# Optimization experiments

Hardware: AMD Instinct MI355X
Metric: run time of the kernel (lower is better)

The kernel has to match this reference:

```python
import jax, jax.numpy as jnp
import numpy as np

EPS = 1e-5  # torch BatchNorm1d default eps


def _bn(y2d, g, b):
    # BatchNorm1d in training mode: biased batch stats over axis 0
    m = y2d.mean(axis=0)
    v = y2d.var(axis=0)
    return (y2d - m) * jax.lax.rsqrt(v + EPS) * g + b


def setup_inputs() -> dict:
    key = jax.random.key(0)
    ks = jax.random.split(key, 18)
    S, B, D, H, O = 1000, 64, 440, 512, 1000
    u = lambda k, shape, n: jax.random.uniform(k, shape, jnp.float32, -1.0 / np.sqrt(n), 1.0 / np.sqrt(n))
    fin = np.sqrt(0.01 / (H + O))
    return {
        "x": jax.random.normal(ks[0], (S, B, D), jnp.float32),
        "Wh": u(ks[1], (H, D), D),
        "Wz": u(ks[2], (H, D), D),
        "Wr": u(ks[3], (H, D), D),
        "Uh": u(ks[4], (H, H), H),
        "Uz": u(ks[5], (H, H), H),
        "Ur": u(ks[6], (H, H), H),
        "gh": 1.0 + 0.1 * jax.random.normal(ks[7], (H,), jnp.float32),
        "bh": 0.1 * jax.random.normal(ks[8], (H,), jnp.float32),
        "gz": 1.0 + 0.1 * jax.random.normal(ks[9], (H,), jnp.float32),
        "bz": 0.1 * jax.random.normal(ks[10], (H,), jnp.float32),
        "gr": 1.0 + 0.1 * jax.random.normal(ks[11], (H,), jnp.float32),
        "br": 0.1 * jax.random.normal(ks[12], (H,), jnp.float32),
        "Wf": jax.random.uniform(ks[13], (O, H), jnp.float32, -fin, fin),
        "gf": 1.0 + 0.1 * jax.random.normal(ks[14], (O,), jnp.float32),
        "bf": 0.1 * jax.random.normal(ks[15], (O,), jnp.float32),
    }


def reference(x, Wh, Wz, Wr, Uh, Uz, Ur, gh, bh, gz, bz, gr, br, Wf, gf, bf):
    S, B, D = x.shape
    H = Wh.shape[0]
    xf = x.reshape(S * B, D)
    # gate input projections (no bias; BN in train mode over flattened (S*B, H))
    wh = _bn(xf @ Wh.T, gh, bh).reshape(S, B, H)
    wz = _bn(xf @ Wz.T, gz, bz).reshape(S, B, H)
    wr = _bn(xf @ Wr.T, gr, br).reshape(S, B, H)

    def step(ht, gates):
        whk, wzk, wrk = gates
        zt = jax.nn.sigmoid(wzk + ht @ Uz.T)
        rt = jax.nn.sigmoid(wrk + ht @ Ur.T)
        hcand = jnp.tanh(whk + (rt * ht) @ Uh.T)  # drop_mask==1 (gru_drop=0.0)
        ht = zt * ht + (1.0 - zt) * hcand
        return ht, ht

    h0 = jnp.zeros((B, H), x.dtype)
    _, h = jax.lax.scan(step, h0, (wh, wz, wr))  # h: (S, B, H)

    ws = _bn(h.reshape(S * B, H) @ Wf.T, gf, bf)
    return jax.nn.log_softmax(ws, axis=1)
```

## Files before the change

### kernel.cpp

```cpp
#include <hip/hip_runtime.h>
#include <cstdint>

typedef unsigned short u16;
typedef __attribute__((ext_vector_type(8))) short bf16x8;
typedef __attribute__((ext_vector_type(4))) float f32x4;

#define S_LEN 1000
#define NWG   32

#define OFF_HALL   0ull
#define SZ_HALL    (1001ull*64*512*2)
#define OFF_WCAT   (OFF_HALL + SZ_HALL)
#define SZ_WCAT    (1536ull*448*2)
#define OFF_WFB    (OFF_WCAT + SZ_WCAT)
#define SZ_WFB     (1024ull*512*2)
#define OFF_RH     (OFF_WFB + SZ_WFB)
#define SZ_RH      (64ull*512*2)
#define OFF_GSUM   (OFF_RH + SZ_RH)
#define OFF_GSQ    (OFF_GSUM + 1536*4)
#define OFF_AALL   (OFF_GSQ  + 1536*4)
#define OFF_CALL   (OFF_AALL + 1536*4)
#define OFF_SSUM   (OFF_CALL + 1536*4)
#define OFF_SSQ    (OFF_SSUM + 1024*4)
#define OFF_AF     (OFF_SSQ  + 1024*4)
#define OFF_CF     (OFF_AF   + 1024*4)
#define OFF_FLAGS  (OFF_CF   + 1024*4)
#define STATS_ZERO_BYTES (OFF_FLAGS + 256 - OFF_GSUM)

__device__ __forceinline__ float bf2f(u16 u) {
  union { unsigned u; float f; } v; v.u = ((unsigned)u) << 16; return v.f;
}
__device__ __forceinline__ u16 f2bf(float f) {
  union { float f; unsigned u; } v; v.f = f;
  unsigned r = (v.u + 0x7fffu + ((v.u >> 16) & 1u)) >> 16;
  return (u16)r;
}
__device__ __forceinline__ float sigm(float x) { return 1.f / (1.f + __expf(-x)); }
__device__ __forceinline__ float tanh_(float x) {
  float e = __expf(-2.f * fabsf(x));
  float r = (1.f - e) / (1.f + e);
  return x >= 0.f ? r : -r;
}

__device__ __forceinline__ void stage16(const u16* g, u16* l) {
#if defined(__has_builtin) && __has_builtin(__builtin_amdgcn_global_load_lds)
  __builtin_amdgcn_global_load_lds((const __attribute__((address_space(1))) unsigned int*)(g),
                                   (__attribute__((address_space(3))) unsigned int*)(l), 16, 0, 0);
#else
  int lane = threadIdx.x & 63;
  *(bf16x8*)(l + lane * 8) = *(const bf16x8*)(g + lane * 0);
#endif
}

__global__ void cvt_pad(const float* __restrict__ src, u16* __restrict__ dst, int incols, int outcols) {
  int r = blockIdx.x, ci = threadIdx.x;
  float v = (ci < incols) ? src[(size_t)r * incols + ci] : 0.f;
  dst[(size_t)r * outcols + ci] = f2bf(v);
}
__global__ void cvt_wf(const float* __restrict__ src, u16* __restrict__ dst) {
  int r = blockIdx.x, ci = threadIdx.x;
  float v = (r < 1000) ? src[(size_t)r * 512 + ci] : 0.f;
  dst[(size_t)r * 512 + ci] = f2bf(v);
}

template<bool F32OUT>
__global__ __launch_bounds__(256, 1) void gemm_bt(const u16* __restrict__ A, const u16* __restrict__ B,
                                                  void* __restrict__ Cout, int K, int ldc, int nlimit) {
  __shared__ __align__(16) u16 smem[16 * 512];
  const int bm = blockIdx.x * 128;
  const int bn = blockIdx.y * 128;
  const int tid = threadIdx.x;
  const int w = tid >> 6;
  const int lane = tid & 63;
  const int r = lane & 15;
  const int q = lane >> 4;
  const int wm = w & 1, wn = w >> 1;

  f32x4 acc[4][4];
#pragma unroll
  for (int i = 0; i < 4; ++i)
#pragma unroll
    for (int j = 0; j < 4; ++j) acc[i][j] = (f32x4){0.f, 0.f, 0.f, 0.f};

  const u16* gA0 = A + (size_t)(bm + w * 16 + r) * K + q * 8;
  const u16* gA1 = A + (size_t)(bm + (w + 4) * 16 + r) * K + q * 8;
  const u16* gB0 = B + (size_t)(bn + w * 16 + r) * K + q * 8;
  const u16* gB1 = B + (size_t)(bn + (w + 4) * 16 + r) * K + q * 8;
  u16* As = smem;
  u16* Bs = smem + 8 * 512;

  for (int k0 = 0; k0 < K; k0 += 32) {
    stage16(gA0 + k0, As + w * 512);
    stage16(gA1 + k0, As + (w + 4) * 512);
    stage16(gB0 + k0, Bs + w * 512);
    stage16(gB1 + k0, Bs + (w + 4) * 512);
    __syncthreads();
    bf16x8 af[4], bf_[4];
#pragma unroll
    for (int mi = 0; mi < 4; ++mi) af[mi] = *(const bf16x8*)(As + (wm * 4 + mi) * 512 + lane * 8);
#pragma unroll
    for (int ni = 0; ni < 4; ++ni) bf_[ni] = *(const bf16x8*)(Bs + (wn * 4 + ni) * 512 + lane * 8);
#pragma unroll
    for (int mi = 0; mi < 4; ++mi)
#pragma unroll
      for (int ni = 0; ni < 4; ++ni)
        acc[mi][ni] = __builtin_amdgcn_mfma_f32_16x16x32_bf16(af[mi], bf_[ni], acc[mi][ni], 0, 0, 0);
    __syncthreads();
  }
  const int row0 = bm + wm * 64;
  const int col0 = bn + wn * 64;
#pragma unroll
  for (int mi = 0; mi < 4; ++mi)
#pragma unroll
    for (int ni = 0; ni < 4; ++ni)
#pragma unroll
      for (int i = 0; i < 4; ++i) {
        int rr = row0 + mi * 16 + q * 4 + i;
        int cc = col0 + ni * 16 + r;
        if (F32OUT) {
          if (cc < nlimit) ((float*)Cout)[(size_t)rr * ldc + cc] = acc[mi][ni][i];
        } else {
          ((u16*)Cout)[(size_t)rr * ldc + cc] = f2bf(acc[mi][ni][i]);
        }
      }
}

template<int BF16IN>
__global__ __launch_bounds__(256, 1) void colstats(const void* __restrict__ Xv, int ld, int ncols,
                                                   float* __restrict__ sum, float* __restrict__ sumsq) {
  const int col = blockIdx.x * 128 + (threadIdx.x & 127);
  const int half = threadIdx.x >> 7;
  const int r0 = blockIdx.y * 2000;
  float s = 0.f, ss = 0.f;
  if (col < ncols) {
    if (BF16IN) {
      const u16* X = (const u16*)Xv;
      for (int rr = r0 + half; rr < r0 + 2000; rr += 2) {
        float v = bf2f(X[(size_t)rr * ld + col]); s += v; ss += v * v;
      }
    } else {
      const float* X = (const float*)Xv;
      for (int rr = r0 + half; rr < r0 + 2000; rr += 2) {
        float v = X[(size_t)rr * ld + col]; s += v; ss += v * v;
      }
    }
  }
  __shared__ float ls[128], lss[128];
  if (half) { ls[threadIdx.x & 127] = s; lss[threadIdx.x & 127] = ss; }
  __syncthreads();
  if (!half && col < ncols) {
    s += ls[threadIdx.x]; ss += lss[threadIdx.x];
    atomicAdd(&sum[col], s); atomicAdd(&sumsq[col], ss);
  }
}

__global__ void fin_gate(const float* __restrict__ sum, const float* __restrict__ sq,
                         const float* gh, const float* bh, const float* gz, const float* bz,
                         const float* gr, const float* br, float* __restrict__ a, float* __restrict__ c) {
  int j = blockIdx.x * 256 + threadIdx.x;
  if (j >= 1536) return;
  float m = sum[j] * (1.f / 64000.f);
  float v = sq[j] * (1.f / 64000.f) - m * m;
  int seg = j >> 9, jj = j & 511;
  float gg = seg == 0 ? gh[jj] : seg == 1 ? gz[jj] : gr[jj];
  float bb = seg == 0 ? bh[jj] : seg == 1 ? bz[jj] : br[jj];
  float aa = gg * rsqrtf(v + 1e-5f);
  a[j] = aa; c[j] = bb - m * aa;
}

__global__ void fin_score(const float* __restrict__ sum, const float* __restrict__ sq,
                          const float* __restrict__ gfp, const float* __restrict__ bfp,
                          float* __restrict__ a, float* __restrict__ c) {
  int j = blockIdx.x * 256 + threadIdx.x;
  if (j >= 1000) return;
  float m = sum[j] * (1.f / 64000.f);
  float v = sq[j] * (1.f / 64000.f) - m * m;
  float aa = gfp[j] * rsqrtf(v + 1e-5f);
  a[j] = aa; c[j] = bfp[j] - m * aa;
}

__device__ __forceinline__ void gbar(unsigned* cnt, unsigned* gen, unsigned n) {
  __syncthreads();
  if (threadIdx.x == 0) {
    __builtin_amdgcn_fence(__ATOMIC_RELEASE, "agent");
    unsigned prev = __hip_atomic_fetch_add(cnt, 1u, __ATOMIC_ACQ_REL, __HIP_MEMORY_SCOPE_AGENT);
    if (prev == n * NWG - 1u) {
      __hip_atomic_store(gen, n, __ATOMIC_RELEASE, __HIP_MEMORY_SCOPE_AGENT);
    } else {
      while (__hip_atomic_load(gen, __ATOMIC_ACQUIRE, __HIP_MEMORY_SCOPE_AGENT) < n)
        __builtin_amdgcn_s_sleep(1);
    }
    __builtin_amdgcn_fence(__ATOMIC_ACQUIRE, "agent");
  }
  __syncthreads();
}

__global__ __launch_bounds__(256, 1) void scan_kernel(
    const u16* __restrict__ gates,
    const float* __restrict__ Uz, const float* __restrict__ Ur, const float* __restrict__ Uh,
    const float* __restrict__ acoef, const float* __restrict__ ccoef,
    u16* __restrict__ hall,
    u16* __restrict__ rh,
    unsigned* __restrict__ bcnt, unsigned* __restrict__ bgen) {
  __shared__ __align__(16) u16 Us[3][16][520];
  __shared__ float co[6][16];
  const int g = blockIdx.x;
  const int j0 = g * 16;
  const int tid = threadIdx.x;
  const int w = tid >> 6;
  const int lane = tid & 63;
  const int r = lane & 15;
  const int q = lane >> 4;

  for (int idx = tid; idx < 3 * 16 * 512; idx += 256) {
    int u = idx >> 13;
    int rem = idx & 8191;
    int j = rem >> 9;
    int k = rem & 511;
    const float* U = (u == 0) ? Uz : (u == 1) ? Ur : Uh;
    Us[u][j][k] = f2bf(U[(size_t)(j0 + j) * 512 + k]);
  }
  if (tid < 16) {
    co[0][tid] = acoef[512 + j0 + tid];  co[1][tid] = ccoef[512 + j0 + tid];
    co[2][tid] = acoef[1024 + j0 + tid]; co[3][tid] = ccoef[1024 + j0 + tid];
    co[4][tid] = acoef[j0 + tid];        co[5][tid] = ccoef[j0 + tid];
  }
  __syncthreads();
  const float az = co[0][r], cz = co[1][r], ar = co[2][r], cr = co[3][r];
  const float ah = co[4][r], ch = co[5][r];

  unsigned bn_ = 0;
  for (int t = 1; t <= S_LEN; ++t) {
    const u16* hprev = hall + (size_t)(t - 1) * (64 * 512);
    f32x4 accz = {0.f, 0.f, 0.f, 0.f}, accr = {0.f, 0.f, 0.f, 0.f};
    const u16* arow = hprev + (size_t)(w * 16 + r) * 512 + q * 8;
#pragma unroll
    for (int ks = 0; ks < 16; ++ks) {
      bf16x8 a = *(const bf16x8*)(arow + ks * 32);
      bf16x8 bz = *(const bf16x8*)(&Us[0][r][ks * 32 + q * 8]);
      bf16x8 br2 = *(const bf16x8*)(&Us[1][r][ks * 32 + q * 8]);
      accz = __builtin_amdgcn_mfma_f32_16x16x32_bf16(a, bz, accz, 0, 0, 0);
      accr = __builtin_amdgcn_mfma_f32_16x16x32_bf16(a, br2, accr, 0, 0, 0);
    }
    const size_t grow = (size_t)(t - 1) * 64 + w * 16 + q * 4;
    float zv[4], rv[4], hp[4];
#pragma unroll
    for (int i = 0; i < 4; ++i) {
      float wz = bf2f(gates[(grow + i) * 1536 + 512 + j0 + r]);
      float wr = bf2f(gates[(grow + i) * 1536 + 1024 + j0 + r]);
      zv[i] = sigm(accz[i] + wz * az + cz);
      rv[i] = sigm(accr[i] + wr * ar + cr);
      hp[i] = bf2f(hprev[(size_t)(w * 16 + q * 4 + i) * 512 + j0 + r]);
      rh[(size_t)(w * 16 + q * 4 + i) * 512 + j0 + r] = f2bf(rv[i] * hp[i]);
    }
    gbar(bcnt, bgen, ++bn_);
    f32x4 acch = {0.f, 0.f, 0.f, 0.f};
    const u16* rrow = rh + (size_t)(w * 16 + r) * 512 + q * 8;
#pragma unroll
    for (int ks = 0; ks < 16; ++ks) {
      bf16x8 a = *(const bf16x8*)(rrow + ks * 32);
      bf16x8 bh = *(const bf16x8*)(&Us[2][r][ks * 32 + q * 8]);
      acch = __builtin_amdgcn_mfma_f32_16x16x32_bf16(a, bh, acch, 0, 0, 0);
    }
    u16* hnew = hall + (size_t)t * (64 * 512);
#pragma unroll
    for (int i = 0; i < 4; ++i) {
      float wh = bf2f(gates[(grow + i) * 1536 + j0 + r]);
      float hc = tanh_(acch[i] + wh * ah + ch);
      float hn = zv[i] * hp[i] + (1.f - zv[i]) * hc;
      hnew[(size_t)(w * 16 + q * 4 + i) * 512 + j0 + r] = f2bf(hn);
    }
    gbar(bcnt, bgen, ++bn_);
  }
}

__global__ __launch_bounds__(256, 1) void logsoftmax_k(float* __restrict__ S,
                                                       const float* __restrict__ a, const float* __restrict__ c) {
  __shared__ float as_[1000], cs_[1000];
  for (int i = threadIdx.x; i < 1000; i += 256) { as_[i] = a[i]; cs_[i] = c[i]; }
  __syncthreads();
  const int w = threadIdx.x >> 6, lane = threadIdx.x & 63;
  for (int it = 0; it < 4; ++it) {
    const int row = blockIdx.x * 16 + it * 4 + w;
    float* Srow = S + (size_t)row * 1000;
    float tv[16];
    float mx = -3.0e38f;
#pragma unroll
    for (int qq = 0; qq < 16; ++qq) {
      int j = lane + qq * 64;
      float v = -3.0e38f;
      if (j < 1000) v = as_[j] * Srow[j] + cs_[j];
      tv[qq] = v;
      mx = fmaxf(mx, v);
    }
#pragma unroll
    for (int o = 32; o > 0; o >>= 1) mx = fmaxf(mx, __shfl_xor(mx, o));
    float sm = 0.f;
#pragma unroll
    for (int qq = 0; qq < 16; ++qq) sm += __expf(tv[qq] - mx);
#pragma unroll
    for (int o = 32; o > 0; o >>= 1) sm += __shfl_xor(sm, o);
    float lse = mx + __logf(sm);
#pragma unroll
    for (int qq = 0; qq < 16; ++qq) {
      int j = lane + qq * 64;
      if (j < 1000) Srow[j] = tv[qq] - lse;
    }
  }
}

extern "C" void kernel_launch(void* const* d_in, const int* in_sizes, int n_in,
                              void* d_out, int out_size, void* d_ws, size_t ws_size,
                              hipStream_t stream) {
  const float* x  = (const float*)d_in[0];
  const float* Wh = (const float*)d_in[1];
  const float* Wz = (const float*)d_in[2];
  const float* Wr = (const float*)d_in[3];
  const float* Uh = (const float*)d_in[4];
  const float* Uz = (const float*)d_in[5];
  const float* Ur = (const float*)d_in[6];
  const float* gh = (const float*)d_in[7];
  const float* bh = (const float*)d_in[8];
  const float* gz = (const float*)d_in[9];
  const float* bz = (const float*)d_in[10];
  const float* gr = (const float*)d_in[11];
  const float* br = (const float*)d_in[12];
  const float* Wf = (const float*)d_in[13];
  const float* gf = (const float*)d_in[14];
  const float* bfp = (const float*)d_in[15];

  uint8_t* ws = (uint8_t*)d_ws;
  u16* hall = (u16*)(ws + OFF_HALL);
  u16* xb   = (u16*)(ws + OFF_HALL);
  u16* wcat = (u16*)(ws + OFF_WCAT);
  u16* wfb  = (u16*)(ws + OFF_WFB);
  u16* rh   = (u16*)(ws + OFF_RH);
  float* gsum = (float*)(ws + OFF_GSUM);
  float* gsq  = (float*)(ws + OFF_GSQ);
  float* aall = (float*)(ws + OFF_AALL);
  float* call = (float*)(ws + OFF_CALL);
  float* ssum = (float*)(ws + OFF_SSUM);
  float* ssq  = (float*)(ws + OFF_SSQ);
  float* af   = (float*)(ws + OFF_AF);
  float* cf   = (float*)(ws + OFF_CF);
  unsigned* flags = (unsigned*)(ws + OFF_FLAGS);

  u16* gates = (u16*)d_out;
  float* scores = (float*)d_out;

  hipMemsetAsync(ws + OFF_GSUM, 0, (size_t)STATS_ZERO_BYTES, stream);

  cvt_pad<<<dim3(64000), dim3(448), 0, stream>>>(x, xb, 440, 448);
  cvt_pad<<<dim3(512), dim3(448), 0, stream>>>(Wh, wcat, 440, 448);
  cvt_pad<<<dim3(512), dim3(448), 0, stream>>>(Wz, wcat + 512 * 448, 440, 448);
  cvt_pad<<<dim3(512), dim3(448), 0, stream>>>(Wr, wcat + 1024 * 448, 440, 448);
  cvt_wf<<<dim3(1024), dim3(512), 0, stream>>>(Wf, wfb);

  gemm_bt<false><<<dim3(500, 12), dim3(256), 0, stream>>>(xb, wcat, (void*)gates, 448, 1536, 1536);

  colstats<1><<<dim3(12, 32), dim3(256), 0, stream>>>((const void*)gates, 1536, 1536, gsum, gsq);
  fin_gate<<<dim3(6), dim3(256), 0, stream>>>(gsum, gsq, gh, bh, gz, bz, gr, br, aall, call);

  hipMemsetAsync(ws + OFF_HALL, 0, (size_t)(64 * 512 * 2), stream);

  scan_kernel<<<dim3(NWG), dim3(256), 0, stream>>>(gates, Uz, Ur, Uh, aall, call, hall, rh,
                                                   flags, flags + 32);

  gemm_bt<true><<<dim3(500, 8), dim3(256), 0, stream>>>(hall + 64 * 512, wfb, (void*)scores, 512, 1000, 1000);

  colstats<0><<<dim3(8, 32), dim3(256), 0, stream>>>((const void*)scores, 1000, 1000, ssum, ssq);
  fin_score<<<dim3(4), dim3(256), 0, stream>>>(ssum, ssq, gf, bfp, af, cf);

  logsoftmax_k<<<dim3(4000), dim3(256), 0, stream>>>(scores, af, cf);
}
```

Measured before the change: 13.64 ms.

## Replace scan grid barrier with per-block flags and transpose gate layout

Swaps the counter-based grid barrier in the recurrent scan for per-workgroup flag publishing: each block writes its own flag and one wavefront polls all 32 flags. h and r*h are now exchanged through relaxed agent-scope atomics, stores are packed in pairs, and the previous h is kept in registers instead of being reloaded. The gate GEMM now writes a transposed gates layout so each lane reads its four timestep gates with one 8-byte load. BN stats for the gates become a row reduction that needs no atomics. The risk is memory-ordering correctness, since relaxed atomics plus s_waitcnt replace explicit fences.

```diff
diff --git a/kernel.cpp b/kernel.cpp
--- a/kernel.cpp
+++ b/kernel.cpp
@@ -2,6 +2,7 @@
 #include <cstdint>
 
 typedef unsigned short u16;
+typedef unsigned long long u64;
 typedef __attribute__((ext_vector_type(8))) short bf16x8;
 typedef __attribute__((ext_vector_type(4))) float f32x4;
 
@@ -25,7 +26,7 @@
 #define OFF_AF     (OFF_SSQ  + 1024*4)
 #define OFF_CF     (OFF_AF   + 1024*4)
 #define OFF_FLAGS  (OFF_CF   + 1024*4)
-#define STATS_ZERO_BYTES (OFF_FLAGS + 256 - OFF_GSUM)
+#define STATS_ZERO_BYTES (OFF_FLAGS + 2048 - OFF_SSUM)
 
 __device__ __forceinline__ float bf2f(u16 u) {
   union { unsigned u; float f; } v; v.u = ((unsigned)u) << 16; return v.f;
@@ -42,14 +43,17 @@
   return x >= 0.f ? r : -r;
 }
 
+__device__ __forceinline__ u64 ld8(const u16* p) {
+  return __hip_atomic_load((const u64*)p, __ATOMIC_RELAXED, __HIP_MEMORY_SCOPE_AGENT);
+}
+__device__ __forceinline__ void st4(u16* p, unsigned v) {
+  __hip_atomic_store((unsigned*)p, v, __ATOMIC_RELAXED, __HIP_MEMORY_SCOPE_AGENT);
+}
+union Frag { u64 q[2]; bf16x8 v; };
+
 __device__ __forceinline__ void stage16(const u16* g, u16* l) {
-#if defined(__has_builtin) && __has_builtin(__builtin_amdgcn_global_load_lds)
   __builtin_amdgcn_global_load_lds((const __attribute__((address_space(1))) unsigned int*)(g),
                                    (__attribute__((address_space(3))) unsigned int*)(l), 16, 0, 0);
-#else
-  int lane = threadIdx.x & 63;
-  *(bf16x8*)(l + lane * 8) = *(const bf16x8*)(g + lane * 0);
-#endif
 }
 
 __global__ void cvt_pad(const float* __restrict__ src, u16* __restrict__ dst, int incols, int outcols) {
@@ -63,7 +67,7 @@
   dst[(size_t)r * 512 + ci] = f2bf(v);
 }
 
-template<bool F32OUT>
+template<int MODE>
 __global__ __launch_bounds__(256, 1) void gemm_bt(const u16* __restrict__ A, const u16* __restrict__ B,
                                                   void* __restrict__ Cout, int K, int ldc, int nlimit) {
   __shared__ __align__(16) u16 smem[16 * 512];
@@ -112,37 +116,52 @@
 #pragma unroll
   for (int mi = 0; mi < 4; ++mi)
 #pragma unroll
-    for (int ni = 0; ni < 4; ++ni)
-#pragma unroll
-      for (int i = 0; i < 4; ++i) {
-        int rr = row0 + mi * 16 + q * 4 + i;
-        int cc = col0 + ni * 16 + r;
-        if (F32OUT) {
-          if (cc < nlimit) ((float*)Cout)[(size_t)rr * ldc + cc] = acc[mi][ni][i];
-        } else {
-          ((u16*)Cout)[(size_t)rr * ldc + cc] = f2bf(acc[mi][ni][i]);
-        }
+    for (int ni = 0; ni < 4; ++ni) {
+      int cc = col0 + ni * 16 + r;
+      int rr = row0 + mi * 16 + q * 4;
+      if (MODE == 1) {
+#pragma unroll
+        for (int i = 0; i < 4; ++i)
+          if (cc < nlimit) ((float*)Cout)[(size_t)(rr + i) * ldc + cc] = acc[mi][ni][i];
+      } else {
+        u64 pk = (u64)f2bf(acc[mi][ni][0]) | ((u64)f2bf(acc[mi][ni][1]) << 16) |
+                 ((u64)f2bf(acc[mi][ni][2]) << 32) | ((u64)f2bf(acc[mi][ni][3]) << 48);
+        *(u64*)((u16*)Cout + (size_t)cc * ldc + rr) = pk;
       }
-}
-
-template<int BF16IN>
-__global__ __launch_bounds__(256, 1) void colstats(const void* __restrict__ Xv, int ld, int ncols,
+    }
+}
+
+__global__ __launch_bounds__(256, 1) void rowstats(const u16* __restrict__ G,
                                                    float* __restrict__ sum, float* __restrict__ sumsq) {
+  const int n = blockIdx.x;
+  const u16* row = G + (size_t)n * 64000;
+  float s = 0.f, ss = 0.f;
+  for (int idx = threadIdx.x * 8; idx < 64000; idx += 2048) {
+    union { bf16x8 v; u16 e[8]; } u;
+    u.v = *(const bf16x8*)(row + idx);
+#pragma unroll
+    for (int e = 0; e < 8; ++e) { float f = bf2f(u.e[e]); s += f; ss += f * f; }
+  }
+#pragma unroll
+  for (int o = 32; o > 0; o >>= 1) { s += __shfl_xor(s, o); ss += __shfl_xor(ss, o); }
+  __shared__ float ls[4], lss[4];
+  if ((threadIdx.x & 63) == 0) { ls[threadIdx.x >> 6] = s; lss[threadIdx.x >> 6] = ss; }
+  __syncthreads();
+  if (threadIdx.x == 0) {
+    sum[n]   = ls[0] + ls[1] + ls[2] + ls[3];
+    sumsq[n] = lss[0] + lss[1] + lss[2] + lss[3];
+  }
+}
+
+__global__ __launch_bounds__(256, 1) void colstats_f32(const float* __restrict__ X, int ld, int ncols,
+                                                       float* __restrict__ sum, float* __restrict__ sumsq) {
   const int col = blockIdx.x * 128 + (threadIdx.x & 127);
   const int half = threadIdx.x >> 7;
   const int r0 = blockIdx.y * 2000;
   float s = 0.f, ss = 0.f;
   if (col < ncols) {
-    if (BF16IN) {
-      const u16* X = (const u16*)Xv;
-      for (int rr = r0 + half; rr < r0 + 2000; rr += 2) {
-        float v = bf2f(X[(size_t)rr * ld + col]); s += v; ss += v * v;
-      }
-    } else {
-      const float* X = (const float*)Xv;
-      for (int rr = r0 + half; rr < r0 + 2000; rr += 2) {
-        float v = X[(size_t)rr * ld + col]; s += v; ss += v * v;
-      }
+    for (int rr = r0 + half; rr < r0 + 2000; rr += 2) {
+      float v = X[(size_t)rr * ld + col]; s += v; ss += v * v;
     }
   }
   __shared__ float ls[128], lss[128];
@@ -179,29 +198,31 @@
   a[j] = aa; c[j] = bfp[j] - m * aa;
 }
 
-__device__ __forceinline__ void gbar(unsigned* cnt, unsigned* gen, unsigned n) {
-  __syncthreads();
-  if (threadIdx.x == 0) {
-    __builtin_amdgcn_fence(__ATOMIC_RELEASE, "agent");
-    unsigned prev = __hip_atomic_fetch_add(cnt, 1u, __ATOMIC_ACQ_REL, __HIP_MEMORY_SCOPE_AGENT);
-    if (prev == n * NWG - 1u) {
-      __hip_atomic_store(gen, n, __ATOMIC_RELEASE, __HIP_MEMORY_SCOPE_AGENT);
-    } else {
-      while (__hip_atomic_load(gen, __ATOMIC_ACQUIRE, __HIP_MEMORY_SCOPE_AGENT) < n)
-        __builtin_amdgcn_s_sleep(1);
-    }
-    __builtin_amdgcn_fence(__ATOMIC_ACQUIRE, "agent");
-  }
-  __syncthreads();
+__device__ __forceinline__ void publish_and_wait(unsigned* flags, int g, unsigned val) {
+  asm volatile("s_waitcnt vmcnt(0)" ::: "memory");
+  __syncthreads();
+  if (threadIdx.x == 0)
+    __hip_atomic_store(&flags[g * 16], val, __ATOMIC_RELAXED, __HIP_MEMORY_SCOPE_AGENT);
+  if (threadIdx.x < 64) {
+    const int l = threadIdx.x;
+    for (;;) {
+      unsigned v = (l < NWG) ? __hip_atomic_load(&flags[l * 16], __ATOMIC_RELAXED, __HIP_MEMORY_SCOPE_AGENT)
+                             : val;
+      if (__all(v >= val)) break;
+      __builtin_amdgcn_s_sleep(1);
+    }
+  }
+  __syncthreads();
+  asm volatile("" ::: "memory");
 }
 
 __global__ __launch_bounds__(256, 1) void scan_kernel(
-    const u16* __restrict__ gates,
+    const u16* __restrict__ gatesT,
     const float* __restrict__ Uz, const float* __restrict__ Ur, const float* __restrict__ Uh,
     const float* __restrict__ acoef, const float* __restrict__ ccoef,
     u16* __restrict__ hall,
     u16* __restrict__ rh,
-    unsigned* __restrict__ bcnt, unsigned* __restrict__ bgen) {
+    unsigned* __restrict__ flags) {
   __shared__ __align__(16) u16 Us[3][16][520];
   __shared__ float co[6][16];
   const int g = blockIdx.x;
@@ -229,48 +250,66 @@
   const float az = co[0][r], cz = co[1][r], ar = co[2][r], cr = co[3][r];
   const float ah = co[4][r], ch = co[5][r];
 
-  unsigned bn_ = 0;
+  const u16* gRowH = gatesT + (size_t)(j0 + r) * 64000;
+  const u16* gRowZ = gatesT + (size_t)(512 + j0 + r) * 64000;
+  const u16* gRowR = gatesT + (size_t)(1024 + j0 + r) * 64000;
+
+  float hp[4] = {0.f, 0.f, 0.f, 0.f};
+
   for (int t = 1; t <= S_LEN; ++t) {
+    const int ct = (t - 1) * 64 + w * 16 + q * 4;
+    const u64 wzq = *(const u64*)(gRowZ + ct);
+    const u64 wrq = *(const u64*)(gRowR + ct);
+    const u64 whq = *(const u64*)(gRowH + ct);
+
     const u16* hprev = hall + (size_t)(t - 1) * (64 * 512);
     f32x4 accz = {0.f, 0.f, 0.f, 0.f}, accr = {0.f, 0.f, 0.f, 0.f};
     const u16* arow = hprev + (size_t)(w * 16 + r) * 512 + q * 8;
 #pragma unroll
     for (int ks = 0; ks < 16; ++ks) {
-      bf16x8 a = *(const bf16x8*)(arow + ks * 32);
+      Frag a; a.q[0] = ld8(arow + ks * 32); a.q[1] = ld8(arow + ks * 32 + 4);
       bf16x8 bz = *(const bf16x8*)(&Us[0][r][ks * 32 + q * 8]);
       bf16x8 br2 = *(const bf16x8*)(&Us[1][r][ks * 32 + q * 8]);
-      accz = __builtin_amdgcn_mfma_f32_16x16x32_bf16(a, bz, accz, 0, 0, 0);
-      accr = __builtin_amdgcn_mfma_f32_16x16x32_bf16(a, br2, accr, 0, 0, 0);
-    }
-    const size_t grow = (size_t)(t - 1) * 64 + w * 16 + q * 4;
-    float zv[4], rv[4], hp[4];
+      accz = __builtin_amdgcn_mfma_f32_16x16x32_bf16(a.v, bz, accz, 0, 0, 0);
+      accr = __builtin_amdgcn_mfma_f32_16x16x32_bf16(a.v, br2, accr, 0, 0, 0);
+    }
+    float zv[4];
 #pragma unroll
     for (int i = 0; i < 4; ++i) {
-      float wz = bf2f(gates[(grow + i) * 1536 + 512 + j0 + r]);
-      float wr = bf2f(gates[(grow + i) * 1536 + 1024 + j0 + r]);
+      float wz = bf2f((u16)(wzq >> (16 * i)));
+      float wr = bf2f((u16)(wrq >> (16 * i)));
       zv[i] = sigm(accz[i] + wz * az + cz);
-      rv[i] = sigm(accr[i] + wr * ar + cr);
-      hp[i] = bf2f(hprev[(size_t)(w * 16 + q * 4 + i) * 512 + j0 + r]);
-      rh[(size_t)(w * 16 + q * 4 + i) * 512 + j0 + r] = f2bf(rv[i] * hp[i]);
-    }
-    gbar(bcnt, bgen, ++bn_);
+      float rv = sigm(accr[i] + wr * ar + cr);
+      u16 rhb = f2bf(rv * hp[i]);
+      float partner = __shfl_xor(bf2f(rhb), 1);
+      if ((r & 1) == 0)
+        st4(rh + (size_t)(w * 16 + q * 4 + i) * 512 + j0 + r,
+            (unsigned)rhb | ((unsigned)f2bf(partner) << 16));
+    }
+    publish_and_wait(flags, g, 2 * t - 1);
+
     f32x4 acch = {0.f, 0.f, 0.f, 0.f};
     const u16* rrow = rh + (size_t)(w * 16 + r) * 512 + q * 8;
 #pragma unroll
     for (int ks = 0; ks < 16; ++ks) {
-      bf16x8 a = *(const bf16x8*)(rrow + ks * 32);
+      Frag a; a.q[0] = ld8(rrow + ks * 32); a.q[1] = ld8(rrow + ks * 32 + 4);
       bf16x8 bh = *(const bf16x8*)(&Us[2][r][ks * 32 + q * 8]);
-      acch = __builtin_amdgcn_mfma_f32_16x16x32_bf16(a, bh, acch, 0, 0, 0);
+      acch = __builtin_amdgcn_mfma_f32_16x16x32_bf16(a.v, bh, acch, 0, 0, 0);
     }
     u16* hnew = hall + (size_t)t * (64 * 512);
 #pragma unroll
     for (int i = 0; i < 4; ++i) {
-      float wh = bf2f(gates[(grow + i) * 1536 + j0 + r]);
+      float wh = bf2f((u16)(whq >> (16 * i)));
       float hc = tanh_(acch[i] + wh * ah + ch);
       float hn = zv[i] * hp[i] + (1.f - zv[i]) * hc;
-      hnew[(size_t)(w * 16 + q * 4 + i) * 512 + j0 + r] = f2bf(hn);
-    }
-    gbar(bcnt, bgen, ++bn_);
+      u16 hb = f2bf(hn);
+      hp[i] = bf2f(hb);
+      float partner = __shfl_xor(hp[i], 1);
+      if ((r & 1) == 0)
+        st4(hnew + (size_t)(w * 16 + q * 4 + i) * 512 + j0 + r,
+            (unsigned)hb | ((unsigned)f2bf(partner) << 16));
+    }
+    publish_and_wait(flags, g, 2 * t);
   }
 }
 
@@ -345,10 +384,10 @@
   float* cf   = (float*)(ws + OFF_CF);
   unsigned* flags = (unsigned*)(ws + OFF_FLAGS);
 
-  u16* gates = (u16*)d_out;
+  u16* gatesT = (u16*)d_out;
   float* scores = (float*)d_out;
 
-  hipMemsetAsync(ws + OFF_GSUM, 0, (size_t)STATS_ZERO_BYTES, stream);
+  hipMemsetAsync(ws + OFF_SSUM, 0, (size_t)STATS_ZERO_BYTES, stream);
 
   cvt_pad<<<dim3(64000), dim3(448), 0, stream>>>(x, xb, 440, 448);
   cvt_pad<<<dim3(512), dim3(448), 0, stream>>>(Wh, wcat, 440, 448);
@@ -356,19 +395,18 @@
   cvt_pad<<<dim3(512), dim3(448), 0, stream>>>(Wr, wcat + 1024 * 448, 440, 448);
   cvt_wf<<<dim3(1024), dim3(512), 0, stream>>>(Wf, wfb);
 
-  gemm_bt<false><<<dim3(500, 12), dim3(256), 0, stream>>>(xb, wcat, (void*)gates, 448, 1536, 1536);
-
-  colstats<1><<<dim3(12, 32), dim3(256), 0, stream>>>((const void*)gates, 1536, 1536, gsum, gsq);
+  gemm_bt<2><<<dim3(500, 12), dim3(256), 0, stream>>>(xb, wcat, (void*)gatesT, 448, 64000, 1536);
+
+  rowstats<<<dim3(1536), dim3(256), 0, stream>>>(gatesT, gsum, gsq);
   fin_gate<<<dim3(6), dim3(256), 0, stream>>>(gsum, gsq, gh, bh, gz, bz, gr, br, aall, call);
 
   hipMemsetAsync(ws + OFF_HALL, 0, (size_t)(64 * 512 * 2), stream);
 
-  scan_kernel<<<dim3(NWG), dim3(256), 0, stream>>>(gates, Uz, Ur, Uh, aall, call, hall, rh,
-                                                   flags, flags + 32);
-
-  gemm_bt<true><<<dim3(500, 8), dim3(256), 0, stream>>>(hall + 64 * 512, wfb, (void*)scores, 512, 1000, 1000);
-
-  colstats<0><<<dim3(8, 32), dim3(256), 0, stream>>>((const void*)scores, 1000, 1000, ssum, ssq);
+  scan_kernel<<<dim3(NWG), dim3(256), 0, stream>>>(gatesT, Uz, Ur, Uh, aall, call, hall, rh, flags);
+
+  gemm_bt<1><<<dim3(500, 8), dim3(256), 0, stream>>>(hall + 64 * 512, wfb, (void*)scores, 512, 1000, 1000);
+
+  colstats_f32<<<dim3(8, 32), dim3(256), 0, stream>>>(scores, 1000, 1000, ssum, ssq);
   fin_score<<<dim3(4), dim3(256), 0, stream>>>(ssum, ssq, gf, bfp, af, cf);
 
   logsoftmax_k<<<dim3(4000), dim3(256), 0, stream>>>(scores, af, cf);
```

Result: faster. 12.51 ms (-8.3%).
